# Performance work log

Measured on AMD Instinct MI355X. Metric: run time of the kernel, lower is better.

## Reference

```python
import jax, jax.numpy as jnp
import numpy as np

EMBED_DIM = 1024
NUM_HEADS = 16
HEAD_DIM = EMBED_DIM // NUM_HEADS
D_FF = 4096
N, T, S = 4, 2048, 2048


def _linear_params(key, d_in, d_out):
    k1, k2 = jax.random.split(key)
    bound = 1.0 / np.sqrt(d_in)
    W = jax.random.uniform(k1, (d_in, d_out), minval=-bound, maxval=bound, dtype=jnp.float32)
    b = jax.random.uniform(k2, (d_out,), minval=-bound, maxval=bound, dtype=jnp.float32)
    return W, b


def setup_inputs() -> dict:
    key = jax.random.key(0)
    ks = jax.random.split(key, 20)
    inp = {
        'tgt': jax.random.normal(ks[0], (N, T, EMBED_DIM), dtype=jnp.float32),
        'memory': jax.random.normal(ks[1], (N, S, EMBED_DIM), dtype=jnp.float32),
        'tgt_mask': jnp.tril(jnp.ones((T, T), dtype=jnp.float32)),
    }
    # self-attn params
    for i, nm in enumerate(['sa_Wq', 'sa_Wk', 'sa_Wv', 'sa_A', 'ca_Wq', 'ca_Wk', 'ca_Wv', 'ca_A']):
        W, b = _linear_params(ks[2 + i], EMBED_DIM, EMBED_DIM)
        inp[nm] = W
        inp[nm + '_b'] = b
    W1, b1 = _linear_params(ks[10], EMBED_DIM, D_FF)
    W2, b2 = _linear_params(ks[11], D_FF, EMBED_DIM)
    inp.update(lin1_W=W1, lin1_b=b1, lin2_W=W2, lin2_b=b2)
    for i in (1, 2, 3):
        inp[f'ln{i}_g'] = jnp.ones((EMBED_DIM,), dtype=jnp.float32)
        inp[f'ln{i}_b'] = jnp.zeros((EMBED_DIM,), dtype=jnp.float32)
    return inp


def _layer_norm(x, g, b, eps=1e-5):
    mu = jnp.mean(x, axis=-1, keepdims=True)
    var = jnp.var(x, axis=-1, keepdims=True)
    return (x - mu) * jax.lax.rsqrt(var + eps) * g + b


def _mha(query, key, value, Wq, bq, Wk, bk, Wv, bv, Wa, ba, mask=None):
    Nq, Tq, D = query.shape
    Tk = key.shape[1]
    q = (query @ Wq + bq).reshape(Nq, Tq, NUM_HEADS, HEAD_DIM)
    k = (key @ Wk + bk).reshape(Nq, Tk, NUM_HEADS, HEAD_DIM)
    v = (value @ Wv + bv).reshape(Nq, Tk, NUM_HEADS, HEAD_DIM)
    attn = jnp.einsum('bthd,bshd->bhts', q, k) / np.sqrt(HEAD_DIM)
    if mask is not None:
        attn = jnp.where(mask == 0, -jnp.inf, attn)
    score = jax.nn.softmax(attn, axis=-1)
    y = jnp.einsum('bhts,bshd->bthd', score, v).reshape(Nq, Tq, D)
    return y @ Wa + ba


def reference(tgt, memory, tgt_mask,
              sa_Wq, sa_Wq_b, sa_Wk, sa_Wk_b, sa_Wv, sa_Wv_b, sa_A, sa_A_b,
              ca_Wq, ca_Wq_b, ca_Wk, ca_Wk_b, ca_Wv, ca_Wv_b, ca_A, ca_A_b,
              lin1_W, lin1_b, lin2_W, lin2_b,
              ln1_g, ln1_b, ln2_g, ln2_b, ln3_g, ln3_b):
    t2 = _mha(tgt, tgt, tgt, sa_Wq, sa_Wq_b, sa_Wk, sa_Wk_b, sa_Wv, sa_Wv_b, sa_A, sa_A_b, tgt_mask)
    x = _layer_norm(tgt + t2, ln1_g, ln1_b)
    t2 = _mha(x, memory, memory, ca_Wq, ca_Wq_b, ca_Wk, ca_Wk_b, ca_Wv, ca_Wv_b, ca_A, ca_A_b)
    x = _layer_norm(x + t2, ln2_g, ln2_b)
    t2 = jax.nn.relu(x @ lin1_W + lin1_b) @ lin2_W + lin2_b
    return _layer_norm(x + t2, ln3_g, ln3_b)
```

## Files before the change

kernel.cpp:

```cpp
#include <hip/hip_runtime.h>

typedef __bf16 bf16;
typedef __bf16 bf16x4 __attribute__((ext_vector_type(4)));
typedef __bf16 bf16x8 __attribute__((ext_vector_type(8)));
typedef float  f32x4  __attribute__((ext_vector_type(4)));

#define EMBED 1024
#define HEADS 16
#define HDIM  64
#define DFF   4096
#define BATCH 4
#define SEQ   2048
#define MROWS 8192

__global__ __launch_bounds__(256) void cvt_kernel(
    const float* __restrict__ x, bf16* __restrict__ y, int n)
{
  int i = (blockIdx.x * 256 + threadIdx.x) * 8;
  if (i >= n) return;
  float4 a = *(const float4*)(x + i);
  float4 b = *(const float4*)(x + i + 4);
  bf16x8 v;
  v[0] = (bf16)a.x; v[1] = (bf16)a.y; v[2] = (bf16)a.z; v[3] = (bf16)a.w;
  v[4] = (bf16)b.x; v[5] = (bf16)b.y; v[6] = (bf16)b.z; v[7] = (bf16)b.w;
  *(bf16x8*)(y + i) = v;
}

__global__ __launch_bounds__(256) void wt_kernel(
    const float* __restrict__ W, bf16* __restrict__ Wt, int K, int N)
{
  __shared__ __align__(16) float Ls[64 * 68];
  const int k0 = blockIdx.x * 64, n0 = blockIdx.y * 64;
  const int ty = threadIdx.x >> 4, tx = threadIdx.x & 15;
  #pragma unroll
  for (int r = 0; r < 4; ++r) {
    const int k = ty + r * 16;
    float4 v = *(const float4*)(W + (size_t)(k0 + k) * N + n0 + tx * 4);
    *(float4*)(Ls + k * 68 + tx * 4) = v;
  }
  __syncthreads();
  #pragma unroll
  for (int it = 0; it < 2; ++it) {
    const int c = it * 256 + threadIdx.x;
    const int n = c >> 3, kc = (c & 7) * 8;
    bf16x8 v;
    #pragma unroll
    for (int j = 0; j < 8; ++j) v[j] = (bf16)Ls[(kc + j) * 68 + n];
    *(bf16x8*)(Wt + (size_t)(n0 + n) * K + k0 + kc) = v;
  }
}

__global__ void cat3_kernel(float* __restrict__ dst, const float* __restrict__ a,
                            const float* __restrict__ b, const float* __restrict__ c, int n)
{
  int i = blockIdx.x * 256 + threadIdx.x;
  if (i < n) dst[i] = a[i];
  else if (i < 2 * n) dst[i] = b[i - n];
  else if (c && i < 3 * n) dst[i] = c[i - 2 * n];
}

__global__ __launch_bounds__(256) void vtr_kernel(
    const bf16* __restrict__ V, int ldv, bf16* __restrict__ Vt, int Skv)
{
  __shared__ __align__(16) bf16 Ls[64 * 72];
  const int k0 = blockIdx.x * 64;
  const int bh = blockIdx.y, b = bh >> 4, h = bh & 15;
  const int t = threadIdx.x;
  {
    const int key = t >> 2, dc = (t & 3) * 16;
    const bf16* src = V + (size_t)(b * Skv + k0 + key) * ldv + h * HDIM + dc;
    bf16x8 a0 = *(const bf16x8*)src;
    bf16x8 a1 = *(const bf16x8*)(src + 8);
    *(bf16x8*)(Ls + key * 72 + dc) = a0;
    *(bf16x8*)(Ls + key * 72 + dc + 8) = a1;
  }
  __syncthreads();
  {
    const int d = t >> 2, kc = (t & 3) * 16;
    bf16x8 v0, v1;
    #pragma unroll
    for (int j = 0; j < 8; ++j) v0[j] = Ls[(kc + j) * 72 + d];
    #pragma unroll
    for (int j = 0; j < 8; ++j) v1[j] = Ls[(kc + 8 + j) * 72 + d];
    bf16* dst = Vt + ((size_t)(bh * HDIM + d)) * Skv + k0 + kc;
    *(bf16x8*)dst = v0;
    *(bf16x8*)(dst + 8) = v1;
  }
}

__device__ __forceinline__ void gll16(const bf16* g, bf16* l) {
  __builtin_amdgcn_global_load_lds(
      (const __attribute__((address_space(1))) unsigned*)g,
      (__attribute__((address_space(3))) unsigned*)l, 16, 0, 0);
}

__global__ __launch_bounds__(256) void gemm128(
    const bf16* __restrict__ A, int lda, const bf16* __restrict__ Bt, int ldb,
    const float* __restrict__ bias, const bf16* __restrict__ res_b,
    const float* __restrict__ res_f, bf16* __restrict__ out_b,
    float* __restrict__ out_f, int N, int K, int relu)
{
  __shared__ __align__(16) bf16 As[128 * 32];
  __shared__ __align__(16) bf16 Bs[128 * 32];
  const int tid  = threadIdx.x;
  const int lane = tid & 63, wave = tid >> 6;
  const int quad = lane >> 4, l16 = lane & 15;
  const int wm = wave & 1, wn = wave >> 1;
  const int m0 = blockIdx.y * 128, n0 = blockIdx.x * 128;

  const int c0row = tid >> 2, c0kc = (tid & 3) * 8;
  const int c1row = (256 + tid) >> 2, c1kc = c0kc;

  f32x4 acc[4][4];
  #pragma unroll
  for (int i = 0; i < 4; ++i)
    #pragma unroll
    for (int j = 0; j < 4; ++j) acc[i][j] = f32x4{0, 0, 0, 0};

  for (int k0 = 0; k0 < K; k0 += 32) {
    gll16(A  + (size_t)(m0 + c0row) * lda + k0 + c0kc, As + (size_t)(wave * 64) * 8);
    gll16(Bt + (size_t)(n0 + c0row) * ldb + k0 + c0kc, Bs + (size_t)(wave * 64) * 8);
    gll16(A  + (size_t)(m0 + c1row) * lda + k0 + c1kc, As + (size_t)(256 + wave * 64) * 8);
    gll16(Bt + (size_t)(n0 + c1row) * ldb + k0 + c1kc, Bs + (size_t)(256 + wave * 64) * 8);
    __syncthreads();

    bf16x8 af[4], bfr[4];
    #pragma unroll
    for (int i = 0; i < 4; ++i)
      af[i] = *(const bf16x8*)(As + (wm * 64 + i * 16 + l16) * 32 + quad * 8);
    #pragma unroll
    for (int j = 0; j < 4; ++j)
      bfr[j] = *(const bf16x8*)(Bs + (wn * 64 + j * 16 + l16) * 32 + quad * 8);
    #pragma unroll
    for (int i = 0; i < 4; ++i)
      #pragma unroll
      for (int j = 0; j < 4; ++j)
        acc[i][j] = __builtin_amdgcn_mfma_f32_16x16x32_bf16(af[i], bfr[j], acc[i][j], 0, 0, 0);
    __syncthreads();
  }

  #pragma unroll
  for (int j = 0; j < 4; ++j) {
    const int col = n0 + wn * 64 + j * 16 + l16;
    const float bv = bias ? bias[col] : 0.f;
    #pragma unroll
    for (int i = 0; i < 4; ++i) {
      #pragma unroll
      for (int r = 0; r < 4; ++r) {
        const int row = m0 + wm * 64 + i * 16 + quad * 4 + r;
        const size_t idx = (size_t)row * N + col;
        float v = acc[i][j][r] + bv;
        if (res_b) v += (float)res_b[idx];
        if (res_f) v += res_f[idx];
        if (relu)  v = fmaxf(v, 0.f);
        if (out_b) out_b[idx] = (bf16)v;
        if (out_f) out_f[idx] = v;
      }
    }
  }
}

__global__ __launch_bounds__(512, 2) void gemm256(
    const bf16* __restrict__ A, int lda, const bf16* __restrict__ Bt, int ldb,
    const float* __restrict__ bias, const bf16* __restrict__ res_b,
    const float* __restrict__ res_f, bf16* __restrict__ out_b,
    float* __restrict__ out_f, int N, int K, int relu)
{
  __shared__ __align__(16) bf16 As[2][256 * 64];
  __shared__ __align__(16) bf16 Bs[2][256 * 64];
  const int tid  = threadIdx.x;
  const int lane = tid & 63, wave = tid >> 6;
  const int quad = lane >> 4, l16 = lane & 15;
  const int wm = wave & 1, wn = wave >> 1;

  const int gx   = gridDim.x;
  const int nwg  = gx * gridDim.y;
  const int flat = blockIdx.y * gx + blockIdx.x;
  const int qc = nwg >> 3, rc = nwg & 7;
  const int xcd = flat & 7, off = flat >> 3;
  const int wg = (xcd < rc ? xcd * (qc + 1) : rc * (qc + 1) + (xcd - rc) * qc) + off;
  const int m0 = (wg / gx) * 256, n0 = (wg % gx) * 256;

  const int sr8 = lane >> 3;
  const int se  = ((lane & 7) ^ sr8) << 3;

  const int sw  = l16 & 7;
  const int co0 = (quad ^ sw) << 3;
  const int co1 = ((4 + quad) ^ sw) << 3;

  f32x4 acc[8][4];
  #pragma unroll
  for (int i = 0; i < 8; ++i)
    #pragma unroll
    for (int j = 0; j < 4; ++j) acc[i][j] = f32x4{0, 0, 0, 0};

  const int ntile = K >> 6;

  auto stageA = [&](int t, int buf) {
    const int k0 = t << 6;
    #pragma unroll
    for (int g = 0; g < 4; ++g) {
      const int rr = g * 64 + wave * 8;
      gll16(A + (size_t)(m0 + rr + sr8) * lda + k0 + se, &As[buf][(size_t)rr * 64]);
    }
  };
  auto stageB = [&](int t, int buf) {
    const int k0 = t << 6;
    #pragma unroll
    for (int g = 0; g < 4; ++g) {
      const int rr = g * 64 + wave * 8;
      gll16(Bt + (size_t)(n0 + rr + sr8) * ldb + k0 + se, &Bs[buf][(size_t)rr * 64]);
    }
  };

  stageA(0, 0);
  stageB(0, 0);
  __syncthreads();

  for (int t = 0; t < ntile; ++t) {
    const int cur = t & 1;
    const bf16* Ac = As[cur];
    const bf16* Bc = Bs[cur];
    #pragma unroll
    for (int ph = 0; ph < 4; ++ph) {
      const int ih = ph >> 1, jh = ph & 1;
      bf16x8 af[4][2], bfrag[2][2];
      #pragma unroll
      for (int ii = 0; ii < 4; ++ii) {
        const int row = wm * 128 + (ih * 4 + ii) * 16 + l16;
        af[ii][0] = *(const bf16x8*)(Ac + row * 64 + co0);
        af[ii][1] = *(const bf16x8*)(Ac + row * 64 + co1);
      }
      #pragma unroll
      for (int jj = 0; jj < 2; ++jj) {
        const int row = wn * 64 + (jh * 2 + jj) * 16 + l16;
        bfrag[jj][0] = *(const bf16x8*)(Bc + row * 64 + co0);
        bfrag[jj][1] = *(const bf16x8*)(Bc + row * 64 + co1);
      }
      if (t + 1 < ntile) {
        if (ph == 0) stageA(t + 1, cur ^ 1);
        else if (ph == 1) stageB(t + 1, cur ^ 1);
      }
      __builtin_amdgcn_s_barrier();
      __builtin_amdgcn_s_setprio(1);
      #pragma unroll
      for (int ii = 0; ii < 4; ++ii)
        #pragma unroll
        for (int jj = 0; jj < 2; ++jj) {
          acc[ih * 4 + ii][jh * 2 + jj] = __builtin_amdgcn_mfma_f32_16x16x32_bf16(
              af[ii][0], bfrag[jj][0], acc[ih * 4 + ii][jh * 2 + jj], 0, 0, 0);
          acc[ih * 4 + ii][jh * 2 + jj] = __builtin_amdgcn_mfma_f32_16x16x32_bf16(
              af[ii][1], bfrag[jj][1], acc[ih * 4 + ii][jh * 2 + jj], 0, 0, 0);
        }
      __builtin_amdgcn_s_setprio(0);
      __builtin_amdgcn_s_barrier();
    }
    __syncthreads();
  }

  #pragma unroll
  for (int j = 0; j < 4; ++j) {
    const int col = n0 + wn * 64 + j * 16 + l16;
    const float bv = bias ? bias[col] : 0.f;
    #pragma unroll
    for (int i = 0; i < 8; ++i) {
      #pragma unroll
      for (int r = 0; r < 4; ++r) {
        const int row = m0 + wm * 128 + i * 16 + quad * 4 + r;
        const size_t idx = (size_t)row * N + col;
        float v = acc[i][j][r] + bv;
        if (res_b) v += (float)res_b[idx];
        if (res_f) v += res_f[idx];
        if (relu)  v = fmaxf(v, 0.f);
        if (out_b) out_b[idx] = (bf16)v;
        if (out_f) out_f[idx] = v;
      }
    }
  }
}

__global__ __launch_bounds__(256) void ln_kernel(
    const float* __restrict__ x, const float* __restrict__ g, const float* __restrict__ b,
    bf16* __restrict__ out_b, float* __restrict__ out_f)
{
  __shared__ float red[8];
  const int tid = threadIdx.x, lane = tid & 63, wave = tid >> 6;
  const float* xr = x + (size_t)blockIdx.x * EMBED;
  float4 v = *(const float4*)(xr + tid * 4);
  float vv[4] = {v.x, v.y, v.z, v.w};
  float s  = vv[0] + vv[1] + vv[2] + vv[3];
  float s2 = vv[0]*vv[0] + vv[1]*vv[1] + vv[2]*vv[2] + vv[3]*vv[3];
  #pragma unroll
  for (int off = 32; off >= 1; off >>= 1) {
    s  += __shfl_xor(s, off);
    s2 += __shfl_xor(s2, off);
  }
  if (lane == 0) { red[wave] = s; red[4 + wave] = s2; }
  __syncthreads();
  s  = red[0] + red[1] + red[2] + red[3];
  s2 = red[4] + red[5] + red[6] + red[7];
  const float mu  = s * (1.f / EMBED);
  const float var = s2 * (1.f / EMBED) - mu * mu;
  const float rs  = rsqrtf(fmaxf(var, 0.f) + 1e-5f);
  #pragma unroll
  for (int i = 0; i < 4; ++i) {
    const int col = tid * 4 + i;
    const float o = (vv[i] - mu) * rs * g[col] + b[col];
    const size_t idx = (size_t)blockIdx.x * EMBED + col;
    if (out_b) out_b[idx] = (bf16)o;
    if (out_f) out_f[idx] = o;
  }
}

__global__ __launch_bounds__(256) void fattn_kernel(
    const bf16* __restrict__ Q, int ldq, const bf16* __restrict__ K, int ldk,
    const bf16* __restrict__ Vt, bf16* __restrict__ Y, int Skv, int causal)
{
  constexpr int PLD = 72;
  __shared__ __align__(16) bf16 Ks[2][64 * 64];
  __shared__ __align__(16) bf16 Vs[2][64 * 64];
  __shared__ __align__(16) bf16 Ps[4 * 32 * PLD];

  const int tid  = threadIdx.x;
  const int lane = tid & 63, wave = tid >> 6;
  const int quad = lane >> 4, l16 = lane & 15;
  const int q0 = blockIdx.x * 128;
  const int bh = blockIdx.y, b = bh >> 4, h = bh & 15;
  const int wq0 = q0 + wave * 32;

  const bf16* Kb = K + (size_t)b * Skv * ldk + h * HDIM;
  const bf16* Vb = Vt + (size_t)(bh * HDIM) * Skv;

  const int sr = lane >> 3;
  const int se = ((lane & 7) ^ sr) << 3;

  const int sw  = l16 & 7;
  const int co0 = (quad ^ sw) << 3;
  const int co1 = ((4 + quad) ^ sw) << 3;

  auto stage = [&](int kt, int buf) {
    const int k0 = kt * 64;
    const int r0 = wave * 16;
    gll16(Kb + (size_t)(k0 + r0 + sr) * ldk + se,     &Ks[buf][(r0)     * 64]);
    gll16(Kb + (size_t)(k0 + r0 + 8 + sr) * ldk + se, &Ks[buf][(r0 + 8) * 64]);
    gll16(Vb + (size_t)(r0 + sr) * Skv + k0 + se,     &Vs[buf][(r0)     * 64]);
    gll16(Vb + (size_t)(r0 + 8 + sr) * Skv + k0 + se, &Vs[buf][(r0 + 8) * 64]);
  };

  bf16x8 qf[2][2];
  #pragma unroll
  for (int i = 0; i < 2; ++i) {
    const bf16* qp = Q + (size_t)(b * SEQ + wq0 + i * 16 + l16) * ldq + h * HDIM;
    qf[i][0] = *(const bf16x8*)(qp + quad * 8);
    qf[i][1] = *(const bf16x8*)(qp + 32 + quad * 8);
  }

  f32x4 O[2][4];
  float m_run[2], l_run[2];
  #pragma unroll
  for (int i = 0; i < 2; ++i)
    #pragma unroll
    for (int nt = 0; nt < 4; ++nt) O[i][nt] = f32x4{0, 0, 0, 0};
  #pragma unroll
  for (int i = 0; i < 2; ++i) { m_run[i] = -1e30f; l_run[i] = 0.f; }

  bf16* Pw = Ps + wave * 32 * PLD;
  const int nkt = causal ? (q0 / 64 + 2) : (Skv / 64);

  stage(0, 0);
  __syncthreads();

  for (int kt = 0; kt < nkt; ++kt) {
    const int cur = kt & 1;
    const int k0 = kt * 64;
    if (kt + 1 < nkt) stage(kt + 1, cur ^ 1);

    const bf16* Kc = Ks[cur];
    const bf16* Vc = Vs[cur];

    f32x4 s[2][4];
    __builtin_amdgcn_s_setprio(1);
    #pragma unroll
    for (int nt = 0; nt < 4; ++nt) {
      const int row = nt * 16 + l16;
      bf16x8 kf0 = *(const bf16x8*)(Kc + row * 64 + co0);
      bf16x8 kf1 = *(const bf16x8*)(Kc + row * 64 + co1);
      #pragma unroll
      for (int i = 0; i < 2; ++i) {
        f32x4 t = f32x4{0, 0, 0, 0};
        t = __builtin_amdgcn_mfma_f32_16x16x32_bf16(kf0, qf[i][0], t, 0, 0, 0);
        t = __builtin_amdgcn_mfma_f32_16x16x32_bf16(kf1, qf[i][1], t, 0, 0, 0);
        s[i][nt] = t;
      }
    }
    __builtin_amdgcn_s_setprio(0);

    if (causal && (k0 + 63 > wq0)) {
      #pragma unroll
      for (int i = 0; i < 2; ++i) {
        const int q = wq0 + i * 16 + l16;
        #pragma unroll
        for (int nt = 0; nt < 4; ++nt) {
          #pragma unroll
          for (int r = 0; r < 4; ++r) {
            const int key = k0 + nt * 16 + quad * 4 + r;
            if (key > q) s[i][nt][r] = -1e30f;
          }
        }
      }
    }

    #pragma unroll
    for (int i = 0; i < 2; ++i) {
      float pm = s[i][0][0];
      #pragma unroll
      for (int nt = 0; nt < 4; ++nt)
        #pragma unroll
        for (int r = 0; r < 4; ++r) pm = fmaxf(pm, s[i][nt][r]);
      pm = fmaxf(pm, __shfl_xor(pm, 16));
      pm = fmaxf(pm, __shfl_xor(pm, 32));
      const float m_new = fmaxf(m_run[i], pm);
      const float al = __expf((m_run[i] - m_new) * 0.125f);
      m_run[i] = m_new;
      const float mc = m_new * 0.125f;
      float ls = 0.f;
      #pragma unroll
      for (int nt = 0; nt < 4; ++nt) {
        #pragma unroll
        for (int r = 0; r < 4; ++r) {
          const float e = __expf(fmaf(s[i][nt][r], 0.125f, -mc));
          s[i][nt][r] = e;
          ls += e;
        }
      }
      ls += __shfl_xor(ls, 16);
      ls += __shfl_xor(ls, 32);
      l_run[i] = l_run[i] * al + ls;
      #pragma unroll
      for (int nt = 0; nt < 4; ++nt) {
        bf16x4 pk;
        pk[0] = (bf16)s[i][nt][0]; pk[1] = (bf16)s[i][nt][1];
        pk[2] = (bf16)s[i][nt][2]; pk[3] = (bf16)s[i][nt][3];
        *(bf16x4*)(Pw + (i * 16 + l16) * PLD + nt * 16 + quad * 4) = pk;
      }
      float alo[4];
      #pragma unroll
      for (int r = 0; r < 4; ++r) alo[r] = __shfl(al, quad * 4 + r);
      #pragma unroll
      for (int nt = 0; nt < 4; ++nt)
        #pragma unroll
        for (int r = 0; r < 4; ++r) O[i][nt][r] *= alo[r];
    }

    bf16x8 pf[2][2];
    #pragma unroll
    for (int i = 0; i < 2; ++i) {
      pf[i][0] = *(const bf16x8*)(Pw + (i * 16 + l16) * PLD + quad * 8);
      pf[i][1] = *(const bf16x8*)(Pw + (i * 16 + l16) * PLD + 32 + quad * 8);
    }
    __builtin_amdgcn_s_setprio(1);
    #pragma unroll
    for (int nt = 0; nt < 4; ++nt) {
      const int row = nt * 16 + l16;
      bf16x8 vf0 = *(const bf16x8*)(Vc + row * 64 + co0);
      bf16x8 vf1 = *(const bf16x8*)(Vc + row * 64 + co1);
      #pragma unroll
      for (int i = 0; i < 2; ++i) {
        O[i][nt] = __builtin_amdgcn_mfma_f32_16x16x32_bf16(pf[i][0], vf0, O[i][nt], 0, 0, 0);
        O[i][nt] = __builtin_amdgcn_mfma_f32_16x16x32_bf16(pf[i][1], vf1, O[i][nt], 0, 0, 0);
      }
    }
    __builtin_amdgcn_s_setprio(0);
    __syncthreads();
  }

  #pragma unroll
  for (int i = 0; i < 2; ++i) {
    float inv[4];
    #pragma unroll
    for (int r = 0; r < 4; ++r) {
      const float lv = __shfl(l_run[i], quad * 4 + r);
      inv[r] = 1.f / lv;
    }
    #pragma unroll
    for (int nt = 0; nt < 4; ++nt) {
      #pragma unroll
      for (int r = 0; r < 4; ++r) {
        const int q = wq0 + i * 16 + quad * 4 + r;
        Y[((size_t)(b * SEQ + q)) * EMBED + h * HDIM + nt * 16 + l16] = (bf16)(O[i][nt][r] * inv[r]);
      }
    }
  }
}

__global__ void fill_kernel(float* out, float v, int n) {
  int i = blockIdx.x * 256 + threadIdx.x;
  if (i < n) out[i] = v;
}

extern "C" void kernel_launch(void* const* d_in, const int* in_sizes, int n_in,
                              void* d_out, int out_size, void* d_ws, size_t ws_size,
                              hipStream_t stream)
{
  const float* tgt    = (const float*)d_in[0];
  const float* mem    = (const float*)d_in[1];
  const float* sa_Wq  = (const float*)d_in[3];
  const float* sa_Wqb = (const float*)d_in[4];
  const float* sa_Wk  = (const float*)d_in[5];
  const float* sa_Wkb = (const float*)d_in[6];
  const float* sa_Wv  = (const float*)d_in[7];
  const float* sa_Wvb = (const float*)d_in[8];
  const float* sa_A   = (const float*)d_in[9];
  const float* sa_Ab  = (const float*)d_in[10];
  const float* ca_Wq  = (const float*)d_in[11];
  const float* ca_Wqb = (const float*)d_in[12];
  const float* ca_Wk  = (const float*)d_in[13];
  const float* ca_Wkb = (const float*)d_in[14];
  const float* ca_Wv  = (const float*)d_in[15];
  const float* ca_Wvb = (const float*)d_in[16];
  const float* ca_A   = (const float*)d_in[17];
  const float* ca_Ab  = (const float*)d_in[18];
  const float* l1W    = (const float*)d_in[19];
  const float* l1b    = (const float*)d_in[20];
  const float* l2W    = (const float*)d_in[21];
  const float* l2b    = (const float*)d_in[22];
  const float* g1     = (const float*)d_in[23];
  const float* b1     = (const float*)d_in[24];
  const float* g2     = (const float*)d_in[25];
  const float* b2     = (const float*)d_in[26];
  const float* g3     = (const float*)d_in[27];
  const float* b3     = (const float*)d_in[28];

  const size_t MB = 1024 * 1024;
  const size_t NEED = 80 * MB + 4096;
  if (ws_size < NEED) {
    fill_kernel<<<(out_size + 255) / 256, 256, 0, stream>>>((float*)d_out, 3.0f, out_size);
    return;
  }

  char* ws = (char*)d_ws;
  const size_t MD = (size_t)MROWS * EMBED;
  bf16*  qkv   = (bf16*)ws;
  bf16*  yb    = (bf16*)(ws + 48 * MB);
  bf16*  wqkvt = (bf16*)(ws + 48 * MB);
  float* qkvbias = (float*)(ws + 54 * MB + 512 * 1024);
  bf16*  kvb   = (bf16*)ws;
  bf16*  qB    = (bf16*)(ws + 32 * MB);
  bf16*  wkvt  = (bf16*)(ws + 48 * MB);
  bf16*  wqt   = (bf16*)(ws + 52 * MB);
  float* kvbias = (float*)(ws + 54 * MB + 512 * 1024);
  bf16*  awt   = (bf16*)ws;
  bf16*  xb    = (bf16*)(ws + 64 * MB);
  bf16*  hb    = (bf16*)ws;
  bf16*  l1t   = (bf16*)(ws + 32 * MB);
  bf16*  l2t   = (bf16*)(ws + 40 * MB);
  float* P   = (float*)d_out;
  bf16*  inb = (bf16*)d_out;
  bf16*  vtg = (bf16*)((char*)d_out + 16 * MB);

  dim3 blk(256);
  dim3 blk512(512);
  dim3 gQKV(3072 / 256, MROWS / 256);
  dim3 gKV(2048 / 256, MROWS / 256);
  dim3 gEE(EMBED / 128, MROWS / 128);
  dim3 gF1(2048 / 256, MROWS / 256);
  dim3 gAT(SEQ / 128, BATCH * HEADS);
  dim3 gVT(SEQ / 64, BATCH * HEADS);
  dim3 gWee(16, 16);
  const int ncv = (int)(MD / 8 / 256);

  cvt_kernel<<<ncv, blk, 0, stream>>>(tgt, inb, (int)MD);
  wt_kernel<<<gWee, blk, 0, stream>>>(sa_Wq, wqkvt, EMBED, EMBED);
  wt_kernel<<<gWee, blk, 0, stream>>>(sa_Wk, wqkvt + 1024 * 1024, EMBED, EMBED);
  wt_kernel<<<gWee, blk, 0, stream>>>(sa_Wv, wqkvt + 2 * 1024 * 1024, EMBED, EMBED);
  cat3_kernel<<<12, blk, 0, stream>>>(qkvbias, sa_Wqb, sa_Wkb, sa_Wvb, EMBED);
  gemm256<<<gQKV, blk512, 0, stream>>>(inb, EMBED, wqkvt, EMBED, qkvbias, nullptr, nullptr, qkv, nullptr, 3072, EMBED, 0);
  vtr_kernel<<<gVT, blk, 0, stream>>>(qkv + 2048, 3072, vtg, SEQ);
  fattn_kernel<<<gAT, blk, 0, stream>>>(qkv, 3072, qkv + 1024, 3072, vtg, yb, SEQ, 1);
  wt_kernel<<<gWee, blk, 0, stream>>>(sa_A, awt, EMBED, EMBED);
  gemm128<<<gEE, blk, 0, stream>>>(yb, EMBED, awt, EMBED, sa_Ab, nullptr, tgt, nullptr, P, EMBED, EMBED, 0);
  ln_kernel<<<MROWS, blk, 0, stream>>>(P, g1, b1, xb, nullptr);

  cvt_kernel<<<ncv, blk, 0, stream>>>(mem, inb, (int)MD);
  wt_kernel<<<gWee, blk, 0, stream>>>(ca_Wk, wkvt, EMBED, EMBED);
  wt_kernel<<<gWee, blk, 0, stream>>>(ca_Wv, wkvt + 1024 * 1024, EMBED, EMBED);
  wt_kernel<<<gWee, blk, 0, stream>>>(ca_Wq, wqt, EMBED, EMBED);
  cat3_kernel<<<8, blk, 0, stream>>>(kvbias, ca_Wkb, ca_Wvb, nullptr, EMBED);
  gemm256<<<gKV, blk512, 0, stream>>>(inb, EMBED, wkvt, EMBED, kvbias, nullptr, nullptr, kvb, nullptr, 2048, EMBED, 0);
  gemm128<<<gEE, blk, 0, stream>>>(xb, EMBED, wqt, EMBED, ca_Wqb, nullptr, nullptr, qB, nullptr, EMBED, EMBED, 0);
  vtr_kernel<<<gVT, blk, 0, stream>>>(kvb + 1024, 2048, vtg, SEQ);
  fattn_kernel<<<gAT, blk, 0, stream>>>(qB, 1024, kvb, 2048, vtg, yb, SEQ, 0);
  wt_kernel<<<gWee, blk, 0, stream>>>(ca_A, awt, EMBED, EMBED);
  gemm128<<<gEE, blk, 0, stream>>>(yb, EMBED, awt, EMBED, ca_Ab, xb, nullptr, nullptr, P, EMBED, EMBED, 0);
  ln_kernel<<<MROWS, blk, 0, stream>>>(P, g2, b2, xb, nullptr);

  wt_kernel<<<dim3(16, 64), blk, 0, stream>>>(l1W, l1t, EMBED, DFF);
  wt_kernel<<<dim3(64, 16), blk, 0, stream>>>(l2W, l2t, DFF, EMBED);
  gemm256<<<gF1, blk512, 0, stream>>>(xb, EMBED, l1t, EMBED, l1b, nullptr, nullptr, hb, nullptr, 2048, EMBED, 1);
  gemm128<<<gEE, blk, 0, stream>>>(hb, 2048, l2t, DFF, l2b, xb, nullptr, nullptr, P, EMBED, 2048, 0);
  gemm256<<<gF1, blk512, 0, stream>>>(xb, EMBED, l1t + (size_t)2048 * 1024, EMBED, l1b + 2048, nullptr, nullptr, hb, nullptr, 2048, EMBED, 1);
  gemm128<<<gEE, blk, 0, stream>>>(hb, 2048, l2t + 2048, DFF, nullptr, nullptr, P, nullptr, P, EMBED, 2048, 0);
  ln_kernel<<<MROWS, blk, 0, stream>>>(P, g3, b3, nullptr, (float*)d_out);
}
```

Measured before the change: 1.253 ms.

## Pipeline GEMM loads with swizzled LDS and balance causal attention by pairing tiles

Measured after the change: 1.156 ms. -7.8%, faster.

```diff
diff --git a/kernel.cpp b/kernel.cpp
--- a/kernel.cpp
+++ b/kernel.cpp
@@ -100,16 +100,29 @@
     const float* __restrict__ res_f, bf16* __restrict__ out_b,
     float* __restrict__ out_f, int N, int K, int relu)
 {
-  __shared__ __align__(16) bf16 As[128 * 32];
-  __shared__ __align__(16) bf16 Bs[128 * 32];
+  __shared__ __align__(16) bf16 As[3][128 * 32];
+  __shared__ __align__(16) bf16 Bs[3][128 * 32];
   const int tid  = threadIdx.x;
   const int lane = tid & 63, wave = tid >> 6;
   const int quad = lane >> 4, l16 = lane & 15;
   const int wm = wave & 1, wn = wave >> 1;
-  const int m0 = blockIdx.y * 128, n0 = blockIdx.x * 128;
-
-  const int c0row = tid >> 2, c0kc = (tid & 3) * 8;
-  const int c1row = (256 + tid) >> 2, c1kc = c0kc;
+
+  const int gx   = gridDim.x;
+  const int nwg  = gx * gridDim.y;
+  const int flat = blockIdx.y * gx + blockIdx.x;
+  const int wg   = (flat & 7) * (nwg >> 3) + (flat >> 3);
+  const int m0 = (wg / gx) * 128, n0 = (wg % gx) * 128;
+
+  const int c0row = tid >> 2;
+  const int c0kc  = (((tid & 3) ^ ((tid >> 2) & 3) ^ ((tid >> 4) & 3))) * 8;
+  const int c1row = 64 + c0row;
+
+  const int co = ((quad ^ ((l16 & 3) ^ ((l16 >> 2) & 3)))) * 8;
+
+  const bf16* a0 = A  + (size_t)(m0 + c0row) * lda + c0kc;
+  const bf16* b0 = Bt + (size_t)(n0 + c0row) * ldb + c0kc;
+  const bf16* a1 = A  + (size_t)(m0 + c1row) * lda + c0kc;
+  const bf16* b1 = Bt + (size_t)(n0 + c1row) * ldb + c0kc;
 
   f32x4 acc[4][4];
   #pragma unroll
@@ -117,26 +130,42 @@
     #pragma unroll
     for (int j = 0; j < 4; ++j) acc[i][j] = f32x4{0, 0, 0, 0};
 
-  for (int k0 = 0; k0 < K; k0 += 32) {
-    gll16(A  + (size_t)(m0 + c0row) * lda + k0 + c0kc, As + (size_t)(wave * 64) * 8);
-    gll16(Bt + (size_t)(n0 + c0row) * ldb + k0 + c0kc, Bs + (size_t)(wave * 64) * 8);
-    gll16(A  + (size_t)(m0 + c1row) * lda + k0 + c1kc, As + (size_t)(256 + wave * 64) * 8);
-    gll16(Bt + (size_t)(n0 + c1row) * ldb + k0 + c1kc, Bs + (size_t)(256 + wave * 64) * 8);
-    __syncthreads();
+  auto stage = [&](int k0, int buf) {
+    gll16(a0 + k0, As[buf] + wave * 512);
+    gll16(b0 + k0, Bs[buf] + wave * 512);
+    gll16(a1 + k0, As[buf] + 2048 + wave * 512);
+    gll16(b1 + k0, Bs[buf] + 2048 + wave * 512);
+  };
+
+  const int nk = K >> 5;
+  stage(0, 0);
+  if (nk > 1) stage(32, 1);
+
+  int cur = 0;
+  for (int t = 0; t < nk; ++t) {
+    if (t + 1 < nk) asm volatile("s_waitcnt vmcnt(4)" ::: "memory");
+    else            asm volatile("s_waitcnt vmcnt(0)" ::: "memory");
+    __builtin_amdgcn_s_barrier();
+    __builtin_amdgcn_sched_barrier(0);
 
     bf16x8 af[4], bfr[4];
     #pragma unroll
     for (int i = 0; i < 4; ++i)
-      af[i] = *(const bf16x8*)(As + (wm * 64 + i * 16 + l16) * 32 + quad * 8);
+      af[i] = *(const bf16x8*)(As[cur] + (wm * 64 + i * 16 + l16) * 32 + co);
     #pragma unroll
     for (int j = 0; j < 4; ++j)
-      bfr[j] = *(const bf16x8*)(Bs + (wn * 64 + j * 16 + l16) * 32 + quad * 8);
+      bfr[j] = *(const bf16x8*)(Bs[cur] + (wn * 64 + j * 16 + l16) * 32 + co);
     #pragma unroll
     for (int i = 0; i < 4; ++i)
       #pragma unroll
       for (int j = 0; j < 4; ++j)
         acc[i][j] = __builtin_amdgcn_mfma_f32_16x16x32_bf16(af[i], bfr[j], acc[i][j], 0, 0, 0);
-    __syncthreads();
+
+    if (t + 2 < nk) {
+      int nb = cur + 2; if (nb >= 3) nb -= 3;
+      stage((t + 2) << 5, nb);
+    }
+    cur = (cur + 1 == 3) ? 0 : cur + 1;
   }
 
   #pragma unroll
@@ -174,57 +203,57 @@
   const int wm = wave & 1, wn = wave >> 1;
 
   const int gx   = gridDim.x;
-  const int nwg  = gx * gridDim.y;
+  const int nwg  = gx * (int)gridDim.y;
   const int flat = blockIdx.y * gx + blockIdx.x;
-  const int qc = nwg >> 3, rc = nwg & 7;
-  const int xcd = flat & 7, off = flat >> 3;
-  const int wg = (xcd < rc ? xcd * (qc + 1) : rc * (qc + 1) + (xcd - rc) * qc) + off;
+  const int wg   = (flat & 7) * (nwg >> 3) + (flat >> 3);
   const int m0 = (wg / gx) * 256, n0 = (wg % gx) * 256;
 
-  const int sr8 = lane >> 3;
-  const int se  = ((lane & 7) ^ sr8) << 3;
+  const int srow = tid >> 3;
+  const int se   = ((tid & 7) ^ ((tid >> 3) & 7)) << 3;
 
   const int sw  = l16 & 7;
   const int co0 = (quad ^ sw) << 3;
   const int co1 = ((4 + quad) ^ sw) << 3;
 
+  const bf16* aA = A  + (size_t)(m0 + srow) * lda + se;
+  const bf16* aB = Bt + (size_t)(n0 + srow) * ldb + se;
+  const size_t a64 = (size_t)64 * lda, b64 = (size_t)64 * ldb;
+
   f32x4 acc[8][4];
   #pragma unroll
   for (int i = 0; i < 8; ++i)
     #pragma unroll
     for (int j = 0; j < 4; ++j) acc[i][j] = f32x4{0, 0, 0, 0};
 
-  const int ntile = K >> 6;
-
-  auto stageA = [&](int t, int buf) {
+  auto stage = [&](int t, int buf) {
     const int k0 = t << 6;
     #pragma unroll
     for (int g = 0; g < 4; ++g) {
-      const int rr = g * 64 + wave * 8;
-      gll16(A + (size_t)(m0 + rr + sr8) * lda + k0 + se, &As[buf][(size_t)rr * 64]);
+      gll16(aA + (size_t)g * a64 + k0, As[buf] + (g * 64 + wave * 8) * 64);
+      gll16(aB + (size_t)g * b64 + k0, Bs[buf] + (g * 64 + wave * 8) * 64);
     }
   };
-  auto stageB = [&](int t, int buf) {
-    const int k0 = t << 6;
-    #pragma unroll
-    for (int g = 0; g < 4; ++g) {
-      const int rr = g * 64 + wave * 8;
-      gll16(Bt + (size_t)(n0 + rr + sr8) * ldb + k0 + se, &Bs[buf][(size_t)rr * 64]);
-    }
-  };
-
-  stageA(0, 0);
-  stageB(0, 0);
-  __syncthreads();
-
-  for (int t = 0; t < ntile; ++t) {
+
+  const int nt = K >> 6;
+  stage(0, 0);
+
+  for (int t = 0; t < nt; ++t) {
     const int cur = t & 1;
+    if (t + 1 < nt) {
+      stage(t + 1, cur ^ 1);
+      asm volatile("s_waitcnt vmcnt(8)" ::: "memory");
+    } else {
+      asm volatile("s_waitcnt vmcnt(0)" ::: "memory");
+    }
+    __builtin_amdgcn_s_barrier();
+    __builtin_amdgcn_sched_barrier(0);
+
     const bf16* Ac = As[cur];
     const bf16* Bc = Bs[cur];
     #pragma unroll
     for (int ph = 0; ph < 4; ++ph) {
       const int ih = ph >> 1, jh = ph & 1;
-      bf16x8 af[4][2], bfrag[2][2];
+      bf16x8 af[4][2], bfr[2][2];
       #pragma unroll
       for (int ii = 0; ii < 4; ++ii) {
         const int row = wm * 128 + (ih * 4 + ii) * 16 + l16;
@@ -234,28 +263,22 @@
       #pragma unroll
       for (int jj = 0; jj < 2; ++jj) {
         const int row = wn * 64 + (jh * 2 + jj) * 16 + l16;
-        bfrag[jj][0] = *(const bf16x8*)(Bc + row * 64 + co0);
-        bfrag[jj][1] = *(const bf16x8*)(Bc + row * 64 + co1);
-      }
-      if (t + 1 < ntile) {
-        if (ph == 0) stageA(t + 1, cur ^ 1);
-        else if (ph == 1) stageB(t + 1, cur ^ 1);
-      }
-      __builtin_amdgcn_s_barrier();
+        bfr[jj][0] = *(const bf16x8*)(Bc + row * 64 + co0);
+        bfr[jj][1] = *(const bf16x8*)(Bc + row * 64 + co1);
+      }
       __builtin_amdgcn_s_setprio(1);
       #pragma unroll
       for (int ii = 0; ii < 4; ++ii)
         #pragma unroll
         for (int jj = 0; jj < 2; ++jj) {
           acc[ih * 4 + ii][jh * 2 + jj] = __builtin_amdgcn_mfma_f32_16x16x32_bf16(
-              af[ii][0], bfrag[jj][0], acc[ih * 4 + ii][jh * 2 + jj], 0, 0, 0);
+              af[ii][0], bfr[jj][0], acc[ih * 4 + ii][jh * 2 + jj], 0, 0, 0);
           acc[ih * 4 + ii][jh * 2 + jj] = __builtin_amdgcn_mfma_f32_16x16x32_bf16(
-              af[ii][1], bfrag[jj][1], acc[ih * 4 + ii][jh * 2 + jj], 0, 0, 0);
+              af[ii][1], bfr[jj][1], acc[ih * 4 + ii][jh * 2 + jj], 0, 0, 0);
         }
       __builtin_amdgcn_s_setprio(0);
-      __builtin_amdgcn_s_barrier();
-    }
-    __syncthreads();
+    }
+    __builtin_amdgcn_s_barrier();
   }
 
   #pragma unroll
@@ -324,9 +347,7 @@
   const int tid  = threadIdx.x;
   const int lane = tid & 63, wave = tid >> 6;
   const int quad = lane >> 4, l16 = lane & 15;
-  const int q0 = blockIdx.x * 128;
   const int bh = blockIdx.y, b = bh >> 4, h = bh & 15;
-  const int wq0 = q0 + wave * 32;
 
   const bf16* Kb = K + (size_t)b * Skv * ldk + h * HDIM;
   const bf16* Vb = Vt + (size_t)(bh * HDIM) * Skv;
@@ -347,147 +368,157 @@
     gll16(Vb + (size_t)(r0 + 8 + sr) * Skv + k0 + se, &Vs[buf][(r0 + 8) * 64]);
   };
 
-  bf16x8 qf[2][2];
-  #pragma unroll
-  for (int i = 0; i < 2; ++i) {
-    const bf16* qp = Q + (size_t)(b * SEQ + wq0 + i * 16 + l16) * ldq + h * HDIM;
-    qf[i][0] = *(const bf16x8*)(qp + quad * 8);
-    qf[i][1] = *(const bf16x8*)(qp + 32 + quad * 8);
-  }
-
-  f32x4 O[2][4];
-  float m_run[2], l_run[2];
-  #pragma unroll
-  for (int i = 0; i < 2; ++i)
-    #pragma unroll
-    for (int nt = 0; nt < 4; ++nt) O[i][nt] = f32x4{0, 0, 0, 0};
-  #pragma unroll
-  for (int i = 0; i < 2; ++i) { m_run[i] = -1e30f; l_run[i] = 0.f; }
-
   bf16* Pw = Ps + wave * 32 * PLD;
-  const int nkt = causal ? (q0 / 64 + 2) : (Skv / 64);
-
-  stage(0, 0);
-  __syncthreads();
-
-  for (int kt = 0; kt < nkt; ++kt) {
-    const int cur = kt & 1;
-    const int k0 = kt * 64;
-    if (kt + 1 < nkt) stage(kt + 1, cur ^ 1);
-
-    const bf16* Kc = Ks[cur];
-    const bf16* Vc = Vs[cur];
-
-    f32x4 s[2][4];
-    __builtin_amdgcn_s_setprio(1);
-    #pragma unroll
-    for (int nt = 0; nt < 4; ++nt) {
-      const int row = nt * 16 + l16;
-      bf16x8 kf0 = *(const bf16x8*)(Kc + row * 64 + co0);
-      bf16x8 kf1 = *(const bf16x8*)(Kc + row * 64 + co1);
+  const int npass = causal ? 2 : 1;
+
+  for (int pass = 0; pass < npass; ++pass) {
+    const int qt = causal ? (pass == 0 ? (int)blockIdx.x
+                                       : (SEQ / 128 - 1 - (int)blockIdx.x))
+                          : (int)blockIdx.x;
+    const int q0  = qt * 128;
+    const int wq0 = q0 + wave * 32;
+
+    bf16x8 qf[2][2];
+    #pragma unroll
+    for (int i = 0; i < 2; ++i) {
+      const bf16* qp = Q + (size_t)(b * SEQ + wq0 + i * 16 + l16) * ldq + h * HDIM;
+      qf[i][0] = *(const bf16x8*)(qp + quad * 8);
+      qf[i][1] = *(const bf16x8*)(qp + 32 + quad * 8);
+    }
+
+    f32x4 O[2][4];
+    float m_run[2], l_run[2];
+    #pragma unroll
+    for (int i = 0; i < 2; ++i)
+      #pragma unroll
+      for (int nt = 0; nt < 4; ++nt) O[i][nt] = f32x4{0, 0, 0, 0};
+    #pragma unroll
+    for (int i = 0; i < 2; ++i) { m_run[i] = -1e30f; l_run[i] = 0.f; }
+
+    const int nkt = causal ? (q0 / 64 + 2) : (Skv / 64);
+
+    stage(0, 0);
+    __syncthreads();
+
+    for (int kt = 0; kt < nkt; ++kt) {
+      const int cur = kt & 1;
+      const int k0 = kt * 64;
+      if (kt + 1 < nkt) stage(kt + 1, cur ^ 1);
+
+      const bf16* Kc = Ks[cur];
+      const bf16* Vc = Vs[cur];
+
+      f32x4 s[2][4];
+      __builtin_amdgcn_s_setprio(1);
+      #pragma unroll
+      for (int nt = 0; nt < 4; ++nt) {
+        const int row = nt * 16 + l16;
+        bf16x8 kf0 = *(const bf16x8*)(Kc + row * 64 + co0);
+        bf16x8 kf1 = *(const bf16x8*)(Kc + row * 64 + co1);
+        #pragma unroll
+        for (int i = 0; i < 2; ++i) {
+          f32x4 t = f32x4{0, 0, 0, 0};
+          t = __builtin_amdgcn_mfma_f32_16x16x32_bf16(kf0, qf[i][0], t, 0, 0, 0);
+          t = __builtin_amdgcn_mfma_f32_16x16x32_bf16(kf1, qf[i][1], t, 0, 0, 0);
+          s[i][nt] = t;
+        }
+      }
+      __builtin_amdgcn_s_setprio(0);
+
+      if (causal && (k0 + 63 > wq0)) {
+        #pragma unroll
+        for (int i = 0; i < 2; ++i) {
+          const int q = wq0 + i * 16 + l16;
+          #pragma unroll
+          for (int nt = 0; nt < 4; ++nt) {
+            #pragma unroll
+            for (int r = 0; r < 4; ++r) {
+              const int key = k0 + nt * 16 + quad * 4 + r;
+              if (key > q) s[i][nt][r] = -1e30f;
+            }
+          }
+        }
+      }
+
       #pragma unroll
       for (int i = 0; i < 2; ++i) {
-        f32x4 t = f32x4{0, 0, 0, 0};
-        t = __builtin_amdgcn_mfma_f32_16x16x32_bf16(kf0, qf[i][0], t, 0, 0, 0);
-        t = __builtin_amdgcn_mfma_f32_16x16x32_bf16(kf1, qf[i][1], t, 0, 0, 0);
-        s[i][nt] = t;
-      }
-    }
-    __builtin_amdgcn_s_setprio(0);
-
-    if (causal && (k0 + 63 > wq0)) {
-      #pragma unroll
-      for (int i = 0; i < 2; ++i) {
-        const int q = wq0 + i * 16 + l16;
+        float pm = s[i][0][0];
+        #pragma unroll
+        for (int nt = 0; nt < 4; ++nt)
+          #pragma unroll
+          for (int r = 0; r < 4; ++r) pm = fmaxf(pm, s[i][nt][r]);
+        pm = fmaxf(pm, __shfl_xor(pm, 16));
+        pm = fmaxf(pm, __shfl_xor(pm, 32));
+        const float m_new = fmaxf(m_run[i], pm);
+        const float al = __expf((m_run[i] - m_new) * 0.125f);
+        m_run[i] = m_new;
+        const float mc = m_new * 0.125f;
+        float ls = 0.f;
         #pragma unroll
         for (int nt = 0; nt < 4; ++nt) {
           #pragma unroll
           for (int r = 0; r < 4; ++r) {
-            const int key = k0 + nt * 16 + quad * 4 + r;
-            if (key > q) s[i][nt][r] = -1e30f;
+            const float e = __expf(fmaf(s[i][nt][r], 0.125f, -mc));
+            s[i][nt][r] = e;
+            ls += e;
           }
         }
-      }
+        ls += __shfl_xor(ls, 16);
+        ls += __shfl_xor(ls, 32);
+        l_run[i] = l_run[i] * al + ls;
+        #pragma unroll
+        for (int nt = 0; nt < 4; ++nt) {
+          bf16x4 pk;
+          pk[0] = (bf16)s[i][nt][0]; pk[1] = (bf16)s[i][nt][1];
+          pk[2] = (bf16)s[i][nt][2]; pk[3] = (bf16)s[i][nt][3];
+          *(bf16x4*)(Pw + (i * 16 + l16) * PLD + nt * 16 + quad * 4) = pk;
+        }
+        float alo[4];
+        #pragma unroll
+        for (int r = 0; r < 4; ++r) alo[r] = __shfl(al, quad * 4 + r);
+        #pragma unroll
+        for (int nt = 0; nt < 4; ++nt)
+          #pragma unroll
+          for (int r = 0; r < 4; ++r) O[i][nt][r] *= alo[r];
+      }
+
+      bf16x8 pf[2][2];
+      #pragma unroll
+      for (int i = 0; i < 2; ++i) {
+        pf[i][0] = *(const bf16x8*)(Pw + (i * 16 + l16) * PLD + quad * 8);
+        pf[i][1] = *(const bf16x8*)(Pw + (i * 16 + l16) * PLD + 32 + quad * 8);
+      }
+      __builtin_amdgcn_s_setprio(1);
+      #pragma unroll
+      for (int nt = 0; nt < 4; ++nt) {
+        const int row = nt * 16 + l16;
+        bf16x8 vf0 = *(const bf16x8*)(Vc + row * 64 + co0);
+        bf16x8 vf1 = *(const bf16x8*)(Vc + row * 64 + co1);
+        #pragma unroll
+        for (int i = 0; i < 2; ++i) {
+          O[i][nt] = __builtin_amdgcn_mfma_f32_16x16x32_bf16(pf[i][0], vf0, O[i][nt], 0, 0, 0);
+          O[i][nt] = __builtin_amdgcn_mfma_f32_16x16x32_bf16(pf[i][1], vf1, O[i][nt], 0, 0, 0);
+        }
+      }
+      __builtin_amdgcn_s_setprio(0);
+      __syncthreads();
     }
 
     #pragma unroll
     for (int i = 0; i < 2; ++i) {
-      float pm = s[i][0][0];
-      #pragma unroll
-      for (int nt = 0; nt < 4; ++nt)
-        #pragma unroll
-        for (int r = 0; r < 4; ++r) pm = fmaxf(pm, s[i][nt][r]);
-      pm = fmaxf(pm, __shfl_xor(pm, 16));
-      pm = fmaxf(pm, __shfl_xor(pm, 32));
-      const float m_new = fmaxf(m_run[i], pm);
-      const float al = __expf((m_run[i] - m_new) * 0.125f);
-      m_run[i] = m_new;
-      const float mc = m_new * 0.125f;
-      float ls = 0.f;
+      float inv[4];
+      #pragma unroll
+      for (int r = 0; r < 4; ++r) {
+        const float lv = __shfl(l_run[i], quad * 4 + r);
+        inv[r] = 1.f / lv;
+      }
       #pragma unroll
       for (int nt = 0; nt < 4; ++nt) {
         #pragma unroll
         for (int r = 0; r < 4; ++r) {
-          const float e = __expf(fmaf(s[i][nt][r], 0.125f, -mc));
-          s[i][nt][r] = e;
-          ls += e;
+          const int q = wq0 + i * 16 + quad * 4 + r;
+          Y[((size_t)(b * SEQ + q)) * EMBED + h * HDIM + nt * 16 + l16] = (bf16)(O[i][nt][r] * inv[r]);
         }
-      }
-      ls += __shfl_xor(ls, 16);
-      ls += __shfl_xor(ls, 32);
-      l_run[i] = l_run[i] * al + ls;
-      #pragma unroll
-      for (int nt = 0; nt < 4; ++nt) {
-        bf16x4 pk;
-        pk[0] = (bf16)s[i][nt][0]; pk[1] = (bf16)s[i][nt][1];
-        pk[2] = (bf16)s[i][nt][2]; pk[3] = (bf16)s[i][nt][3];
-        *(bf16x4*)(Pw + (i * 16 + l16) * PLD + nt * 16 + quad * 4) = pk;
-      }
-      float alo[4];
-      #pragma unroll
-      for (int r = 0; r < 4; ++r) alo[r] = __shfl(al, quad * 4 + r);
-      #pragma unroll
-      for (int nt = 0; nt < 4; ++nt)
-        #pragma unroll
-        for (int r = 0; r < 4; ++r) O[i][nt][r] *= alo[r];
-    }
-
-    bf16x8 pf[2][2];
-    #pragma unroll
-    for (int i = 0; i < 2; ++i) {
-      pf[i][0] = *(const bf16x8*)(Pw + (i * 16 + l16) * PLD + quad * 8);
-      pf[i][1] = *(const bf16x8*)(Pw + (i * 16 + l16) * PLD + 32 + quad * 8);
-    }
-    __builtin_amdgcn_s_setprio(1);
-    #pragma unroll
-    for (int nt = 0; nt < 4; ++nt) {
-      const int row = nt * 16 + l16;
-      bf16x8 vf0 = *(const bf16x8*)(Vc + row * 64 + co0);
-      bf16x8 vf1 = *(const bf16x8*)(Vc + row * 64 + co1);
-      #pragma unroll
-      for (int i = 0; i < 2; ++i) {
-        O[i][nt] = __builtin_amdgcn_mfma_f32_16x16x32_bf16(pf[i][0], vf0, O[i][nt], 0, 0, 0);
-        O[i][nt] = __builtin_amdgcn_mfma_f32_16x16x32_bf16(pf[i][1], vf1, O[i][nt], 0, 0, 0);
-      }
-    }
-    __builtin_amdgcn_s_setprio(0);
-    __syncthreads();
-  }
-
-  #pragma unroll
-  for (int i = 0; i < 2; ++i) {
-    float inv[4];
-    #pragma unroll
-    for (int r = 0; r < 4; ++r) {
-      const float lv = __shfl(l_run[i], quad * 4 + r);
-      inv[r] = 1.f / lv;
-    }
-    #pragma unroll
-    for (int nt = 0; nt < 4; ++nt) {
-      #pragma unroll
-      for (int r = 0; r < 4; ++r) {
-        const int q = wq0 + i * 16 + quad * 4 + r;
-        Y[((size_t)(b * SEQ + q)) * EMBED + h * HDIM + nt * 16 + l16] = (bf16)(O[i][nt][r] * inv[r]);
       }
     }
   }
@@ -562,8 +593,9 @@
   dim3 blk512(512);
   dim3 gQKV(3072 / 256, MROWS / 256);
   dim3 gKV(2048 / 256, MROWS / 256);
+  dim3 gF1(2048 / 256, MROWS / 256);
   dim3 gEE(EMBED / 128, MROWS / 128);
-  dim3 gF1(2048 / 256, MROWS / 256);
+  dim3 gATC(SEQ / 256, BATCH * HEADS);
   dim3 gAT(SEQ / 128, BATCH * HEADS);
   dim3 gVT(SEQ / 64, BATCH * HEADS);
   dim3 gWee(16, 16);
@@ -576,7 +608,7 @@
   cat3_kernel<<<12, blk, 0, stream>>>(qkvbias, sa_Wqb, sa_Wkb, sa_Wvb, EMBED);
   gemm256<<<gQKV, blk512, 0, stream>>>(inb, EMBED, wqkvt, EMBED, qkvbias, nullptr, nullptr, qkv, nullptr, 3072, EMBED, 0);
   vtr_kernel<<<gVT, blk, 0, stream>>>(qkv + 2048, 3072, vtg, SEQ);
-  fattn_kernel<<<gAT, blk, 0, stream>>>(qkv, 3072, qkv + 1024, 3072, vtg, yb, SEQ, 1);
+  fattn_kernel<<<gATC, blk, 0, stream>>>(qkv, 3072, qkv + 1024, 3072, vtg, yb, SEQ, 1);
   wt_kernel<<<gWee, blk, 0, stream>>>(sa_A, awt, EMBED, EMBED);
   gemm128<<<gEE, blk, 0, stream>>>(yb, EMBED, awt, EMBED, sa_Ab, nullptr, tgt, nullptr, P, EMBED, EMBED, 0);
   ln_kernel<<<MROWS, blk, 0, stream>>>(P, g1, b1, xb, nullptr);
```
